# Performance work log

Measured on AMD Instinct MI355X. Metric: run time of the kernel, lower is better.

The kernel has to match this reference:

```python
import jax, jax.numpy as jnp
import numpy as np

B, H, W, F_HEX, F_GLB = 2, 48, 48, 150, 7
D, NH, L, DF, M = 512, 8, 4, 2048, 128
MAX_W, MAX_H, ATK, REC = 48, 48, 8, 20
S = H * W
DK = D // NH


def _ln(x, g, b):
    m = jnp.mean(x, -1, keepdims=True)
    v = jnp.mean(jnp.square(x - m), -1, keepdims=True)
    return (x - m) * jax.lax.rsqrt(v + 1e-5) * g + b


def _mha(q, k, v, wq, bq, wk, bk, wv, bv, wo, bo, mask=None):
    Bq, Sq, _ = q.shape
    Sk = k.shape[1]
    Q = (q @ wq + bq).reshape(Bq, Sq, NH, DK)
    K = (k @ wk + bk).reshape(Bq, Sk, NH, DK)
    V = (v @ wv + bv).reshape(Bq, Sk, NH, DK)
    s = jnp.einsum('bqhd,bkhd->bhqk', Q, K) / np.float32(np.sqrt(DK))
    if mask is not None:
        s = jnp.where(mask == 0, jnp.float32(-1e9), s)
    a = jax.nn.softmax(s, -1)
    o = jnp.einsum('bhqk,bkhd->bqhd', a, V).reshape(Bq, Sq, D)
    return o @ wo + bo


def setup_inputs():
    key = jax.random.key(0)
    ks = iter(jax.random.split(key, 64))
    w = lambda *sh: jax.random.normal(next(ks), sh, jnp.float32) * 0.02
    z = lambda *sh: jnp.zeros(sh, jnp.float32)
    o = lambda *sh: jnp.ones(sh, jnp.float32)
    return dict(
        map_representation=jax.random.normal(next(ks), (B, H, W, F_HEX), jnp.float32),
        global_features=jax.random.normal(next(ks), (B, F_GLB), jnp.float32),
        memory=jax.random.normal(next(ks), (B, M, D), jnp.float32),
        fog_mask=jax.random.randint(next(ks), (B, H, W), 0, 2, jnp.int32),
        hex_w=w(F_HEX, D), hex_b=z(D), glob_w=w(F_GLB, D), glob_b=z(D),
        mem_wq=w(D, D), mem_bq=z(D), mem_wk=w(D, D), mem_bk=z(D),
        mem_wv=w(D, D), mem_bv=z(D), mem_wo=w(D, D), mem_bo=z(D),
        gate_w=w(2 * D, D), gate_b=z(D),
        mn1_g=o(D), mn1_b=z(D), mn2_g=o(D), mn2_b=z(D),
        lw_q=w(L, D, D), lb_q=z(L, D), lw_k=w(L, D, D), lb_k=z(L, D),
        lw_v=w(L, D, D), lb_v=z(L, D), lw_o=w(L, D, D), lb_o=z(L, D),
        ln1_g=o(L, D), ln1_b=z(L, D), ln2_g=o(L, D), ln2_b=z(L, D),
        ff1_w=w(L, D, DF), ff1_b=z(L, DF), ff2_w=w(L, DF, D), ff2_b=z(L, D),
        pool_w=w(D, 1), pool_b=z(1),
        sx_w=w(D, MAX_W), sx_b=z(MAX_W), sy_w=w(D, MAX_H), sy_b=z(MAX_H),
        tx_w=w(D, MAX_W), tx_b=z(MAX_W), ty_w=w(D, MAX_H), ty_b=z(MAX_H),
        atk_w=w(D, ATK), atk_b=z(ATK), rec_w=w(D, REC), rec_b=z(REC),
        et_w=w(D, 1), et_b=z(1), val_w=w(D, 1), val_b=z(1),
    )


def reference(map_representation, global_features, memory, fog_mask,
              hex_w, hex_b, glob_w, glob_b,
              mem_wq, mem_bq, mem_wk, mem_bk, mem_wv, mem_bv, mem_wo, mem_bo,
              gate_w, gate_b, mn1_g, mn1_b, mn2_g, mn2_b,
              lw_q, lb_q, lw_k, lb_k, lw_v, lb_v, lw_o, lb_o,
              ln1_g, ln1_b, ln2_g, ln2_b, ff1_w, ff1_b, ff2_w, ff2_b,
              pool_w, pool_b, sx_w, sx_b, sy_w, sy_b, tx_w, tx_b, ty_w, ty_b,
              atk_w, atk_b, rec_w, rec_b, et_w, et_b, val_w, val_b):
    # project hex + global features, flatten map to token sequence [B,S,D]
    hexf = map_representation @ hex_w + hex_b
    glob = global_features @ glob_w + glob_b
    seq = (hexf + glob[:, None, None, :]).reshape(B, S, D)
    am = fog_mask.reshape(B, S)[:, None, None, :]  # key mask [B,1,1,S]

    # memory module: cross-attn conditioning + gated memory update (shared MHA weights)
    mem_out = _mha(seq, memory, memory, mem_wq, mem_bq, mem_wk, mem_bk, mem_wv, mem_bv, mem_wo, mem_bo)
    x = _ln(seq + mem_out, mn1_g, mn1_b)
    mem_upd = _mha(memory, seq, seq, mem_wq, mem_bq, mem_wk, mem_bk, mem_wv, mem_bv, mem_wo, mem_bo)
    gate = jax.nn.sigmoid(jnp.concatenate([memory, mem_upd], -1) @ gate_w + gate_b)
    new_memory = _ln(gate * mem_upd + (1.0 - gate) * memory, mn2_g, mn2_b)

    def block(xc, p):
        wq, bq, wk, bk, wv, bv, wo, bo, g1, b1, g2, b2, f1w, f1b, f2w, f2b = p
        att = _mha(xc, xc, xc, wq, bq, wk, bk, wv, bv, wo, bo, mask=am)
        xc = _ln(xc + att, g1, b1)
        h = jax.nn.gelu(xc @ f1w + f1b, approximate=False) @ f2w + f2b
        return _ln(xc + h, g2, b2), None

    x, _ = jax.lax.scan(block, x, (lw_q, lb_q, lw_k, lb_k, lw_v, lb_v, lw_o, lb_o,
                                   ln1_g, ln1_b, ln2_g, ln2_b, ff1_w, ff1_b, ff2_w, ff2_b))

    # attention pooling over tokens
    pw = jax.nn.softmax((x @ pool_w + pool_b)[..., 0], -1)  # [B,S]
    pooled = jnp.einsum('bs,bsd->bd', pw, x)

    return (pooled @ sx_w + sx_b, pooled @ sy_w + sy_b,
            pooled @ tx_w + tx_b, pooled @ ty_w + ty_b,
            pooled @ atk_w + atk_b, pooled @ rec_w + rec_b,
            pooled @ et_w + et_b, pooled @ val_w + val_b, new_memory)
```

## Files before the change

### kernel.cpp

```cpp
#include <hip/hip_runtime.h>
#include <hip/hip_bf16.h>

typedef __hip_bfloat16 bf16;
typedef unsigned short u16;
typedef __attribute__((ext_vector_type(8))) short short8;
typedef __attribute__((ext_vector_type(4))) float f32x4;

__device__ inline float b2f(u16 u){ unsigned int x = ((unsigned int)u) << 16; float f; __builtin_memcpy(&f, &x, 4); return f; }
__device__ inline u16 f2bits(float f){ __hip_bfloat16 h = __float2bfloat16(f); u16 u; __builtin_memcpy(&u, &h, 2); return u; }
__device__ inline void unpk(unsigned int w, float& a, float& b){ a = b2f((u16)(w & 0xffffu)); b = b2f((u16)(w >> 16)); }

__device__ __forceinline__ unsigned int pkbf(float a, float b)
{
  unsigned int ua = __float_as_uint(a) + 0x8000u;
  unsigned int ub = __float_as_uint(b) + 0x8000u;
  return __builtin_amdgcn_perm(ub, ua, 0x07060302u);
}

__global__ __launch_bounds__(512) void detect_k(const unsigned int* __restrict__ raw, int* __restrict__ flag)
{
  __shared__ int cnt;
  if (threadIdx.x == 0) cnt = 0;
  __syncthreads();
  unsigned int w = raw[threadIdx.x];
// ... 45 lines not shown
#pragma unroll
    for (int j = 0; j < 8; j++) o8[j] = f2bits(v[j]);
    __builtin_memcpy(&ov, o8, 16);
  }
  *(uint4*)((u16*)dst + gid) = ov;
}

__global__ __launch_bounds__(256) void gemm_k(
    const bf16* __restrict__ A, int lda, long long sAb, long long sAh,
    const bf16* __restrict__ B, int ldb, long long sBb, long long sBh,
    bf16* __restrict__ C, int ldc, long long sCb, long long sCh,
    int M, int N, int K, int HZ,
    const bf16* __restrict__ bias,
    const bf16* __restrict__ res, int ldres,
    const float* __restrict__ extra, int extraDiv,
    float alpha, int mode)
{
  __shared__ u16 As[64][40];
  __shared__ u16 Bs[64][40];
  int z = blockIdx.z;
  int bz = z / HZ, hz = z - bz * HZ;
  A += (size_t)bz * sAb + (size_t)hz * sAh;
  B += (size_t)bz * sBb + (size_t)hz * sBh;
  C += (size_t)bz * sCb + (size_t)hz * sCh;

  int m0 = blockIdx.y * 64, n0 = blockIdx.x * 64;
  int t = threadIdx.x;
  int r = t >> 2, c0 = (t & 3) << 3;
  int lane = t & 63, wv = t >> 6, lr = lane & 15, lq = lane >> 4;

  f32x4 acc[4];
#pragma unroll
  for (int i = 0; i < 4; i++) acc[i] = (f32x4){0.f, 0.f, 0.f, 0.f};

  const u16* Ag = (const u16*)A;
  const u16* Bg = (const u16*)B;
  bool aok = (m0 + r < M), bok = (n0 + r < N);
  const u16* arow = Ag + (size_t)(m0 + r) * lda + c0;
  const u16* brow = Bg + (size_t)(n0 + r) * ldb + c0;

  uint4 av = {0u,0u,0u,0u}, bv = {0u,0u,0u,0u};
  if (aok) av = *(const uint4*)(arow);
  if (bok) bv = *(const uint4*)(brow);

  for (int kt = 0; kt < K; kt += 32) {
    __syncthreads();
    *(uint4*)&As[r][c0] = av;
    *(uint4*)&Bs[r][c0] = bv;
    uint4 av2 = {0u,0u,0u,0u}, bv2 = {0u,0u,0u,0u};
    int nk = kt + 32;
    if (nk < K) {
      if (aok) av2 = *(const uint4*)(arow + nk);
      if (bok) bv2 = *(const uint4*)(brow + nk);
    }
    __syncthreads();
    short8 af = *(const short8*)&As[wv * 16 + lr][lq * 8];
#pragma unroll
    for (int nt = 0; nt < 4; nt++) {
      short8 bfr = *(const short8*)&Bs[nt * 16 + lr][lq * 8];
      acc[nt] = __builtin_amdgcn_mfma_f32_16x16x32_bf16(af, bfr, acc[nt], 0, 0, 0);
    }
    av = av2; bv = bv2;
  }

#pragma unroll
  for (int nt = 0; nt < 4; nt++) {
    int nn = n0 + nt * 16 + lr;
    if (nn >= N) continue;
    float bb = bias ? (float)bias[nn] : 0.f;
#pragma unroll
    for (int rr = 0; rr < 4; rr++) {
      int mm = m0 + wv * 16 + lq * 4 + rr;
      if (mm >= M) continue;
      float v = acc[nt][rr] * alpha + bb;
      if (mode == 1)      v += extra[(mm / extraDiv) * 512 + nn];
      else if (mode == 2) v = 0.5f * v * (1.f + erff(v * 0.70710678118654752f));
      else if (mode == 4) v += (float)res[(size_t)mm * ldres + nn];
      else if (mode == 5) v = 1.f / (1.f + expf(-v));
      C[(size_t)mm * ldc + nn] = __float2bfloat16(v);
    }
  }
}

__device__ __forceinline__ int swz(int row, int cg)
{
  return row * 64 + ((cg ^ (row & 3) ^ (((row >> 3) & 1) << 2)) << 3);
}

__global__ __launch_bounds__(256) void flash_k(
    const bf16* __restrict__ Qp, long long sQb,
    const bf16* __restrict__ Kp, long long sKb,
    const bf16* __restrict__ VTp, long long sVz,
    float* __restrict__ oAcc, long long sOb,
    float* __restrict__ lAcc, int Ml,
    const int* __restrict__ fog,
    int tilesPerSplit, int SkLen)
{
  __shared__ u16 Kl[64 * 64];
  __shared__ u16 Vl[64 * 64];
  __shared__ float fgl[2304];

  const float SC = 0.125f * 1.44269504088896340736f;
  int z = blockIdx.y, b = z >> 3, h = z & 7;
  int qt = blockIdx.x;
  int kt0 = blockIdx.z * tilesPerSplit;
  int t = threadIdx.x, lane = t & 63, w = t >> 6;
  int lr = lane & 15, lq = lane >> 4;

  const u16* Qg = (const u16*)Qp + (size_t)b * sQb + h * 64;
  const u16* Kg = (const u16*)Kp + (size_t)b * sKb + h * 64;
  const u16* Vg = (const u16*)VTp + (size_t)z * sVz;

  if (fog) {
    for (int j = t; j < SkLen; j += 256) fgl[j] = fog[b * 2304 + j] ? 0.f : -1e30f;
  }

  int qrow = qt * 64 + w * 16 + lr;
  short8 qf0, qf1;
  {
    union { short8 s; u16 u[8]; } i0, i1, o0, o1;
    i0.s = *(const short8*)(Qg + (size_t)qrow * 512 + lq * 8);
    i1.s = *(const short8*)(Qg + (size_t)qrow * 512 + 32 + lq * 8);
#pragma unroll
    for (int j = 0; j < 8; j++) {
      o0.u[j] = f2bits(b2f(i0.u[j]) * SC);
      o1.u[j] = f2bits(b2f(i1.u[j]) * SC);
    }
    qf0 = o0.s; qf1 = o1.s;
  }

  int rowA[4], kAd0[4], kAd1[4];
#pragma unroll
  for (int nt = 0; nt < 4; nt++) {
    rowA[nt] = 32 * (nt >> 1) + 8 * (lr >> 2) + 4 * (nt & 1) + (lr & 3);
    kAd0[nt] = swz(rowA[nt], lq);
    kAd1[nt] = swz(rowA[nt], lq + 4);
  }
  int vAd0[4], vAd1[4];
#pragma unroll
  for (int dt = 0; dt < 4; dt++) {
    vAd0[dt] = swz(dt * 16 + lr, lq);
    vAd1[dt] = swz(dt * 16 + lr, lq + 4);
  }

  f32x4 o[4];
#pragma unroll
  for (int i = 0; i < 4; i++) o[i] = (f32x4){0.f, 0.f, 0.f, 0.f};
  float lsum = 0.f;

  int rr = t >> 2, cg = t & 3, cs = cg * 8;
  int wAd0 = swz(rr, cg), wAd1 = swz(rr, cg + 4);
  for (int kti = 0; kti < tilesPerSplit; kti++) {
    int kt = kt0 + kti;
    __syncthreads();
    const u16* krow = Kg + (size_t)(kt * 64 + rr) * 512;
    const u16* vrow = Vg + (size_t)rr * SkLen + kt * 64;
    *(uint4*)&Kl[wAd0] = *(const uint4*)(krow + cs);
    *(uint4*)&Kl[wAd1] = *(const uint4*)(krow + cs + 32);
    *(uint4*)&Vl[wAd0] = *(const uint4*)(vrow + cs);
    *(uint4*)&Vl[wAd1] = *(const uint4*)(vrow + cs + 32);
    __syncthreads();

    f32x4 s[4];
#pragma unroll
    for (int nt = 0; nt < 4; nt++) {
      s[nt] = (f32x4){0.f, 0.f, 0.f, 0.f};
      short8 kf0 = *(const short8*)&Kl[kAd0[nt]];
      short8 kf1 = *(const short8*)&Kl[kAd1[nt]];
      s[nt] = __builtin_amdgcn_mfma_f32_16x16x32_bf16(kf0, qf0, s[nt], 0, 0, 0);
      s[nt] = __builtin_amdgcn_mfma_f32_16x16x32_bf16(kf1, qf1, s[nt], 0, 0, 0);
    }
    if (fog) {
#pragma unroll
      for (int nt = 0; nt < 4; nt++) {
        int key = kt * 64 + 32 * (nt >> 1) + 8 * lq + 4 * (nt & 1);
        f32x4 mo4 = *(const f32x4*)&fgl[key];
        s[nt] += mo4;
      }
    }
    union { unsigned int u[4]; short8 s8; } pk0, pk1;
#pragma unroll
    for (int nt = 0; nt < 4; nt++) {
      float p0 = exp2f(s[nt][0]), p1 = exp2f(s[nt][1]);
      float p2 = exp2f(s[nt][2]), p3 = exp2f(s[nt][3]);
      lsum += (p0 + p1) + (p2 + p3);
      unsigned int w0 = pkbf(p0, p1);
      unsigned int w1 = pkbf(p2, p3);
      if (nt < 2) { pk0.u[(nt & 1) * 2] = w0; pk0.u[(nt & 1) * 2 + 1] = w1; }
      else        { pk1.u[(nt & 1) * 2] = w0; pk1.u[(nt & 1) * 2 + 1] = w1; }
    }
#pragma unroll
    for (int dt = 0; dt < 4; dt++) {
      short8 vf0 = *(const short8*)&Vl[vAd0[dt]];
      short8 vf1 = *(const short8*)&Vl[vAd1[dt]];
      o[dt] = __builtin_amdgcn_mfma_f32_16x16x32_bf16(pk0.s8, vf0, o[dt], 0, 0, 0);
      o[dt] = __builtin_amdgcn_mfma_f32_16x16x32_bf16(pk1.s8, vf1, o[dt], 0, 0, 0);
    }
  }

  lsum += __shfl_xor(lsum, 16);
  lsum += __shfl_xor(lsum, 32);
  if (lq == 0) atomicAdd(&lAcc[z * Ml + qt * 64 + w * 16 + lr], lsum);

  float* ob = oAcc + (size_t)b * sOb;
  int qb = qt * 64 + w * 16 + lq * 4;
#pragma unroll
  for (int dt = 0; dt < 4; dt++)
#pragma unroll
    for (int r2 = 0; r2 < 4; r2++)
      atomicAdd(&ob[(size_t)(qb + r2) * 512 + h * 64 + dt * 16 + lr], o[dt][r2]);
}

__global__ __launch_bounds__(256) void fdiv_k(const float* __restrict__ oAcc,
                                              const float* __restrict__ lAcc,
                                              int Mq, int Ml, int rows,
                                              bf16* __restrict__ out)
{
  int i = blockIdx.x * 256 + threadIdx.x;
  if (i >= rows * 512) return;
  int row = i >> 9, col = i & 511;
  int b = row / Mq, q = row - b * Mq;
  int zz = b * 8 + (col >> 6);
  float l = lAcc[zz * Ml + q];
  float v = (l > 0.f) ? oAcc[i] / l : 0.f;
  out[i] = __float2bfloat16(v);
}

__global__ __launch_bounds__(256) void transpose_k(const bf16* __restrict__ in, bf16* __restrict__ out,
                                                   int R, int C, int Rpad, long long inB, long long outB)
{
  __shared__ u16 tile[32][33];
  const u16* ip = (const u16*)in + (size_t)blockIdx.z * inB;
  u16* op = (u16*)out + (size_t)blockIdx.z * outB;
  int c0 = blockIdx.x * 32, r0 = blockIdx.y * 32;
  int tx = threadIdx.x & 31, ty = threadIdx.x >> 5;
#pragma unroll
  for (int j = 0; j < 4; j++) {
    int rr = r0 + ty + j * 8, cc = c0 + tx;
    u16 v = 0;
    if (rr < R && cc < C) v = ip[(size_t)rr * C + cc];
    tile[ty + j * 8][tx] = v;
  }
  __syncthreads();
#pragma unroll
  for (int j = 0; j < 4; j++) {
    int oc = c0 + ty + j * 8;
    if (oc < C && r0 + tx < Rpad) op[(size_t)oc * Rpad + r0 + tx] = tile[tx][ty + j * 8];
  }
}

__global__ __launch_bounds__(256) void headT_k(const bf16* __restrict__ in, bf16* __restrict__ out,
                                               int Sk, int rowbase, int bstride)
{
  __shared__ u16 tile[32][33];
  int z = blockIdx.z, b = z >> 3, h = z & 7;
  const u16* ip = (const u16*)in + ((size_t)(rowbase + b * bstride)) * 512 + h * 64;
  u16* op = (u16*)out + (size_t)z * 64 * Sk;
  int r0 = blockIdx.x * 32, c0 = blockIdx.y * 32;
  int tx = threadIdx.x & 31, ty = threadIdx.x >> 5;
#pragma unroll
  for (int j = 0; j < 4; j++)
    tile[ty + j * 8][tx] = ip[(size_t)(r0 + ty + j * 8) * 512 + c0 + tx];
  __syncthreads();
#pragma unroll
  for (int j = 0; j < 4; j++)
    op[(size_t)(c0 + ty + j * 8) * Sk + r0 + tx] = tile[tx][ty + j * 8];
}

__global__ __launch_bounds__(64) void ln_k(const bf16* __restrict__ in, const bf16* __restrict__ g,
                                           const bf16* __restrict__ bb, bf16* __restrict__ out)
{
  size_t row = blockIdx.x; int lane = threadIdx.x;
  const u16* ip = (const u16*)in + row * 512 + lane * 8;
  uint4 rv = *(const uint4*)ip;
  float v[8];
  unpk(rv.x, v[0], v[1]); unpk(rv.y, v[2], v[3]); unpk(rv.z, v[4], v[5]); unpk(rv.w, v[6], v[7]);
  float s = 0.f, s2 = 0.f;
#pragma unroll
  for (int k = 0; k < 8; k++) { s += v[k]; s2 += v[k] * v[k]; }
#pragma unroll
  for (int o = 32; o; o >>= 1) { s += __shfl_xor(s, o); s2 += __shfl_xor(s2, o); }
  float mean = s * (1.f / 512.f);
  float var = s2 * (1.f / 512.f) - mean * mean;
  float rstd = rsqrtf(var + 1e-5f);
  uint4 gv = *(const uint4*)((const u16*)g + lane * 8);
  uint4 bv = *(const uint4*)((const u16*)bb + lane * 8);
  float gf[8], bf2[8];
  unpk(gv.x, gf[0], gf[1]); unpk(gv.y, gf[2], gf[3]); unpk(gv.z, gf[4], gf[5]); unpk(gv.w, gf[6], gf[7]);
  unpk(bv.x, bf2[0], bf2[1]); unpk(bv.y, bf2[2], bf2[3]); unpk(bv.z, bf2[4], bf2[5]); unpk(bv.w, bf2[6], bf2[7]);
  u16 o8[8];
#pragma unroll
  for (int k = 0; k < 8; k++) o8[k] = f2bits((v[k] - mean) * rstd * gf[k] + bf2[k]);
  uint4 ov;
  ov.x = o8[0] | ((unsigned)o8[1] << 16); ov.y = o8[2] | ((unsigned)o8[3] << 16);
  ov.z = o8[4] | ((unsigned)o8[5] << 16); ov.w = o8[6] | ((unsigned)o8[7] << 16);
  *(uint4*)((u16*)out + row * 512 + lane * 8) = ov;
}

__global__ void glob_k(const bf16* __restrict__ gf, const bf16* __restrict__ gw,
                       const bf16* __restrict__ gb, float* __restrict__ out)
{
  int i = blockIdx.x * 256 + threadIdx.x; if (i >= 1024) return;
  int b = i >> 9, d = i & 511;
  float s = (float)gb[d];
#pragma unroll
  for (int f = 0; f < 7; f++) s += (float)gf[b * 7 + f] * (float)gw[f * 512 + d];
  out[i] = s;
}

__global__ void padA_k(const bf16* __restrict__ in, bf16* __restrict__ out)
{
  int i = blockIdx.x * 256 + threadIdx.x; if (i >= 4608 * 160) return;
  int r = i / 160, c = i - r * 160;
  out[i] = (c < 150) ? in[r * 150 + c] : __float2bfloat16(0.f);
}

__global__ void catg_k(const bf16* __restrict__ mem, const bf16* __restrict__ mu, bf16* __restrict__ out)
{
  int i = blockIdx.x * 256 + threadIdx.x; if (i >= 256 * 1024) return;
  int r = i >> 10, c = i & 1023;
  out[i] = (c < 512) ? mem[r * 512 + c] : mu[r * 512 + c - 512];
}

__global__ void gcomb_k(const bf16* __restrict__ g, const bf16* __restrict__ mu,
                        const bf16* __restrict__ mem, bf16* __restrict__ out)
{
  int i = blockIdx.x * 256 + threadIdx.x; if (i >= 131072) return;
  float gg = (float)g[i];
  out[i] = __float2bfloat16(gg * (float)mu[i] + (1.f - gg) * (float)mem[i]);
}

__global__ __launch_bounds__(64) void plog_k(const bf16* __restrict__ x, const bf16* __restrict__ pw,
                                             const bf16* __restrict__ pb, float* __restrict__ out)
{
  size_t row = blockIdx.x; int lane = threadIdx.x;
  uint4 xv = *(const uint4*)((const u16*)x + row * 512 + lane * 8);
  uint4 wv = *(const uint4*)((const u16*)pw + lane * 8);
  float v[8], w[8];
  unpk(xv.x, v[0], v[1]); unpk(xv.y, v[2], v[3]); unpk(xv.z, v[4], v[5]); unpk(xv.w, v[6], v[7]);
  unpk(wv.x, w[0], w[1]); unpk(wv.y, w[2], w[3]); unpk(wv.z, w[4], w[5]); unpk(wv.w, w[6], w[7]);
  float s = 0.f;
#pragma unroll
  for (int k = 0; k < 8; k++) s += v[k] * w[k];
#pragma unroll
  for (int o = 32; o; o >>= 1) s += __shfl_xor(s, o);
  if (lane == 0) out[row] = s + (float)pb[0];
}

__global__ __launch_bounds__(256) void psm_k(const float* __restrict__ lg, float* __restrict__ pw)
{
  __shared__ float red[4];
  int b = blockIdx.x, tid = threadIdx.x;
  const float* p = lg + b * 2304;
  float vals[9]; float mx = -3e38f;
#pragma unroll
// ... 158 lines not shown
  bf16* tLo = (bf16*)alloc(4 * 512 * 512, 2);
  bf16* tF1 = (bf16*)alloc(4ULL * 2048 * 512, 2);
  bf16* tF2 = (bf16*)alloc(4ULL * 512 * 2048, 2);
  float* globF = (float*)alloc(1024, 4);
  bf16* catX = (bf16*)alloc((size_t)CATROW * 512, 2);
  bf16* Qc = (bf16*)alloc((size_t)CATROW * 512, 2);
  bf16* Kc = (bf16*)alloc((size_t)CATROW * 512, 2);
  bf16* Vc = (bf16*)alloc((size_t)CATROW * 512, 2);
  bf16* VmemT = (bf16*)alloc(16ULL * 64 * 128, 2);
  bf16* VsT = (bf16*)alloc(16ULL * 64 * S, 2);
  bf16* mo = (bf16*)alloc((size_t)NROW * 512, 2);
  bf16* tmp1 = (bf16*)alloc((size_t)NROW * 512, 2);
  bf16* xbuf = (bf16*)alloc((size_t)NROW * 512, 2);
  bf16* x2buf = (bf16*)alloc((size_t)NROW * 512, 2);
  bf16* mu0 = (bf16*)alloc(256 * 512, 2);
  bf16* mup = (bf16*)alloc(256 * 512, 2);
  bf16* catg = (bf16*)alloc(256 * 1024, 2);
  bf16* gateb = (bf16*)alloc(256 * 512, 2);
  bf16* nmpre = (bf16*)alloc(256 * 512, 2);
  bf16* nmout = (bf16*)alloc(256 * 512, 2);
  float* plog = (float*)alloc(NROW, 4);
  float* pwv = (float*)alloc(NROW, 4);
  float* pooledF = (float*)alloc(1024, 4);
  float* oAcc = (float*)alloc((size_t)NROW * 512, 4);
  float* lAcc = (float*)alloc(16 * 2304, 4);
  bf16* hbuf = (bf16*)alloc((size_t)NROW * 2048, 2);
  if (off > ws_size) return;

  detect_k<<<1, 512, 0, stream>>>((const unsigned int*)d_in[0], dflag);
  cvtall8_k<<<(coffi / 8 + 255) / 256, 256, 0, stream>>>(ca, canon, dflag);

  auto T = [&](int t) -> const bf16* { return canon + cum[t]; };
  const bf16* map_rep = T(0);
  const bf16* gfeat   = T(1);
  const bf16* memin   = T(2);
  const bf16* hex_w = T(3);  const bf16* hex_b = T(4);
  const bf16* glob_w = T(5); const bf16* glob_b = T(6);
  const bf16* mem_wq = T(7);  const bf16* mem_bq = T(8);
  const bf16* mem_wk = T(9);  const bf16* mem_bk = T(10);
  const bf16* mem_wv = T(11); const bf16* mem_bv = T(12);
  const bf16* mem_wo = T(13); const bf16* mem_bo = T(14);
  const bf16* gate_w = T(15); const bf16* gate_b = T(16);
  const bf16* mn1_g = T(17); const bf16* mn1_b = T(18);
  const bf16* mn2_g = T(19); const bf16* mn2_b = T(20);
  const bf16* lw_q = T(21); const bf16* lb_q = T(22);
  const bf16* lw_k = T(23); const bf16* lb_k = T(24);
  const bf16* lw_v = T(25); const bf16* lb_v = T(26);
  const bf16* lw_o = T(27); const bf16* lb_o = T(28);
  const bf16* ln1_g = T(29); const bf16* ln1_b = T(30);
  const bf16* ln2_g = T(31); const bf16* ln2_b = T(32);
  const bf16* ff1_w = T(33); const bf16* ff1_b = T(34);
  const bf16* ff2_w = T(35); const bf16* ff2_b = T(36);
  const bf16* pool_w = T(37); const bf16* pool_b = T(38);

  transp(stream, hex_w, tHex, 150, 512, 160, 0, 0, 1);
  transp(stream, mem_wq, tWq, 512, 512, 512, 0, 0, 1);
  transp(stream, mem_wk, tWk, 512, 512, 512, 0, 0, 1);
  transp(stream, mem_wv, tWv, 512, 512, 512, 0, 0, 1);
  transp(stream, mem_wo, tWo, 512, 512, 512, 0, 0, 1);
  transp(stream, gate_w, tGate, 1024, 512, 1024, 0, 0, 1);
  transp(stream, lw_q, tLq, 512, 512, 512, 262144, 262144, 4);
  transp(stream, lw_k, tLk, 512, 512, 512, 262144, 262144, 4);
  transp(stream, lw_v, tLv, 512, 512, 512, 262144, 262144, 4);
  transp(stream, lw_o, tLo, 512, 512, 512, 262144, 262144, 4);
  transp(stream, ff1_w, tF1, 512, 2048, 512, 1048576, 1048576, 4);
  transp(stream, ff2_w, tF2, 2048, 512, 2048, 1048576, 1048576, 4);

  glob_k<<<4, 256, 0, stream>>>(gfeat, glob_w, glob_b, globF);
  padA_k<<<(NROW * 160 + 255) / 256, 256, 0, stream>>>(map_rep, aPad);
  gemm(stream, aPad, 160, 0, 0, tHex, 160, 0, 0, catX, 512, 0, 0,
       NROW, 512, 160, 1, 1, hex_b, nullptr, 0, globF, S, 1.f, 1);
  hipMemcpyAsync(catX + (size_t)NROW * 512, memin, 256 * 512 * 2, hipMemcpyDeviceToDevice, stream);

  gemm(stream, catX, 512, 0, 0, tWq, 512, 0, 0, Qc, 512, 0, 0, CATROW, 512, 512, 1, 1, mem_bq, nullptr, 0, nullptr, 1, 1.f, 0);
  gemm(stream, catX, 512, 0, 0, tWk, 512, 0, 0, Kc, 512, 0, 0, CATROW, 512, 512, 1, 1, mem_bk, nullptr, 0, nullptr, 1, 1.f, 0);
  gemm(stream, catX, 512, 0, 0, tWv, 512, 0, 0, Vc, 512, 0, 0, CATROW, 512, 512, 1, 1, mem_bv, nullptr, 0, nullptr, 1, 1.f, 0);

  headT_k<<<dim3(4, 2, 16), 256, 0, stream>>>(Vc, VmemT, 128, NROW, 128);
  hipMemsetAsync(oAcc, 0, (size_t)NROW * 512 * 4, stream);
  hipMemsetAsync(lAcc, 0, 16 * 2304 * 4, stream);
  flash_k<<<dim3(36, 16, 1), 256, 0, stream>>>(Qc, RS, Kc + (size_t)NROW * 512, 128 * 512,
                                               VmemT, 64 * 128, oAcc, RS, lAcc, 2304,
                                               nullptr, 2, 128);
  fdiv_k<<<(NROW * 512 + 255) / 256, 256, 0, stream>>>(oAcc, lAcc, 2304, 2304, NROW, mo);
  gemm(stream, mo, 512, 0, 0, tWo, 512, 0, 0, tmp1, 512, 0, 0,
       NROW, 512, 512, 1, 1, mem_bo, catX, 512, nullptr, 1, 1.f, 4);
  ln_k<<<NROW, 64, 0, stream>>>(tmp1, mn1_g, mn1_b, xbuf);

  headT_k<<<dim3(72, 2, 16), 256, 0, stream>>>(Vc, VsT, S, 0, S);
  hipMemsetAsync(oAcc, 0, 256 * 512 * 4, stream);
  hipMemsetAsync(lAcc, 0, 16 * 128 * 4, stream);
  flash_k<<<dim3(2, 16, 6), 256, 0, stream>>>(Qc + (size_t)NROW * 512, 128 * 512, Kc, RS,
                                              VsT, 64LL * S, oAcc, 128 * 512, lAcc, 128,
                                              nullptr, 6, S);
  fdiv_k<<<(256 * 512 + 255) / 256, 256, 0, stream>>>(oAcc, lAcc, 128, 128, 256, mu0);
  gemm(stream, mu0, 512, 0, 0, tWo, 512, 0, 0, mup, 512, 0, 0,
       256, 512, 512, 1, 1, mem_bo, nullptr, 0, nullptr, 1, 1.f, 0);
  catg_k<<<(256 * 1024 + 255) / 256, 256, 0, stream>>>(memin, mup, catg);
  gemm(stream, catg, 1024, 0, 0, tGate, 1024, 0, 0, gateb, 512, 0, 0,
       256, 512, 1024, 1, 1, gate_b, nullptr, 0, nullptr, 1, 1.f, 5);
  gcomb_k<<<(131072 + 255) / 256, 256, 0, stream>>>(gateb, mup, memin, nmpre);
  ln_k<<<256, 64, 0, stream>>>(nmpre, mn2_g, mn2_b, nmout);
  outstore_k<<<(131072 + 255) / 256, 256, 0, stream>>>(nmout, d_out, dflag);

  for (int l = 0; l < 4; l++) {
    gemm(stream, xbuf, 512, 0, 0, tLq + (size_t)l * 262144, 512, 0, 0, Qc, 512, 0, 0,
         NROW, 512, 512, 1, 1, lb_q + l * 512, nullptr, 0, nullptr, 1, 1.f, 0);
    gemm(stream, xbuf, 512, 0, 0, tLk + (size_t)l * 262144, 512, 0, 0, Kc, 512, 0, 0,
         NROW, 512, 512, 1, 1, lb_k + l * 512, nullptr, 0, nullptr, 1, 1.f, 0);
    gemm(stream, xbuf, 512, 0, 0, tLv + (size_t)l * 262144, 512, 0, 0, Vc, 512, 0, 0,
         NROW, 512, 512, 1, 1, lb_v + l * 512, nullptr, 0, nullptr, 1, 1.f, 0);
    headT_k<<<dim3(72, 2, 16), 256, 0, stream>>>(Vc, VsT, S, 0, S);
    hipMemsetAsync(oAcc, 0, (size_t)NROW * 512 * 4, stream);
    hipMemsetAsync(lAcc, 0, 16 * 2304 * 4, stream);
    flash_k<<<dim3(36, 16, 2), 256, 0, stream>>>(Qc, RS, Kc, RS, VsT, 64LL * S,
                                                 oAcc, RS, lAcc, 2304, fog, 18, S);
    fdiv_k<<<(NROW * 512 + 255) / 256, 256, 0, stream>>>(oAcc, lAcc, 2304, 2304, NROW, mo);
    gemm(stream, mo, 512, 0, 0, tLo + (size_t)l * 262144, 512, 0, 0, tmp1, 512, 0, 0,
         NROW, 512, 512, 1, 1, lb_o + l * 512, xbuf, 512, nullptr, 1, 1.f, 4);
    ln_k<<<NROW, 64, 0, stream>>>(tmp1, ln1_g + l * 512, ln1_b + l * 512, x2buf);
    gemm(stream, x2buf, 512, 0, 0, tF1 + (size_t)l * 1048576, 512, 0, 0, hbuf, 2048, 0, 0,
         NROW, 2048, 512, 1, 1, ff1_b + l * 2048, nullptr, 0, nullptr, 1, 1.f, 2);
    gemm(stream, hbuf, 2048, 0, 0, tF2 + (size_t)l * 1048576, 2048, 0, 0, tmp1, 512, 0, 0,
         NROW, 512, 2048, 1, 1, ff2_b + l * 512, x2buf, 512, nullptr, 1, 1.f, 4);
    ln_k<<<NROW, 64, 0, stream>>>(tmp1, ln2_g + l * 512, ln2_b + l * 512, xbuf);
  }

  plog_k<<<NROW, 64, 0, stream>>>(xbuf, pool_w, pool_b, plog);
  psm_k<<<2, 256, 0, stream>>>(plog, pwv);
  hipMemsetAsync(pooledF, 0, 1024 * sizeof(float), stream);
  pool1_k<<<dim3(36, 2), 256, 0, stream>>>(pwv, xbuf, pooledF);

  heads_k<<<2, 256, 0, stream>>>(pooledF,
      T(39), T(40), T(41), T(42), T(43), T(44), T(45), T(46),
      T(47), T(48), T(49), T(50), T(51), T(52), T(53), T(54),
      d_out, dflag);
}
```

Baseline: 1.252 ms.

## Add 128x128 register-prefetch FFN1 GEMM, bitmask fog, MFMA row sums, vectorized fdiv/LN

Adds a 128x128-tile bf16 MFMA GEMM that prefetches the next K-slab into registers while the current one is computed, and uses it for the FFN1 projection with fused GELU. The flash kernel now applies the fog mask by ANDing the packed bf16 probabilities with a 16-bit mask instead of adding -1e30 to the logits. It also computes the softmax denominator with an extra MFMA against a ones vector instead of scalar adds and shuffles. The division kernel handles four elements per thread with a reciprocal, and layernorm packs four rows per 256-thread block. The new GEMM assumes M, N and K are multiples of 128 and 32, and the row sums now use bf16-rounded probabilities.

```diff
diff --git a/kernel.cpp b/kernel.cpp
--- a/kernel.cpp
+++ b/kernel.cpp
@@ -151,6 +151,84 @@
   }
 }
 
+__global__ __launch_bounds__(256) void gemm128p_k(
+    const bf16* __restrict__ A, int lda,
+    const bf16* __restrict__ B, int ldb,
+    bf16* __restrict__ C, int ldc, int K,
+    const bf16* __restrict__ bias,
+    const bf16* __restrict__ res, int ldres,
+    const float* __restrict__ extra, int extraDiv,
+    float alpha, int mode)
+{
+  __shared__ u16 As[128][40];
+  __shared__ u16 Bs[128][40];
+  int t = threadIdx.x, lane = t & 63, w = t >> 6;
+  int m0 = blockIdx.y * 128, n0 = blockIdx.x * 128;
+  int wm = (w & 1) * 64, wn = (w >> 1) * 64;
+  int lr = lane & 15, lq = lane >> 4;
+  int r = t >> 2, c0 = (t & 3) << 3;
+
+  const u16* Ag = (const u16*)A;
+  const u16* Bg = (const u16*)B;
+  const u16* ar0 = Ag + (size_t)(m0 + r) * lda + c0;
+  const u16* ar1 = Ag + (size_t)(m0 + 64 + r) * lda + c0;
+  const u16* br0 = Bg + (size_t)(n0 + r) * ldb + c0;
+  const u16* br1 = Bg + (size_t)(n0 + 64 + r) * ldb + c0;
+
+  uint4 a0 = *(const uint4*)ar0, a1 = *(const uint4*)ar1;
+  uint4 b0 = *(const uint4*)br0, b1 = *(const uint4*)br1;
+
+  f32x4 acc[4][4];
+#pragma unroll
+  for (int i = 0; i < 4; i++)
+#pragma unroll
+    for (int j = 0; j < 4; j++) acc[i][j] = (f32x4){0.f, 0.f, 0.f, 0.f};
+
+  for (int kt = 0; kt < K; kt += 32) {
+    __syncthreads();
+    *(uint4*)&As[r][c0] = a0;
+    *(uint4*)&As[64 + r][c0] = a1;
+    *(uint4*)&Bs[r][c0] = b0;
+    *(uint4*)&Bs[64 + r][c0] = b1;
+    int nk = kt + 32;
+    if (nk < K) {
+      a0 = *(const uint4*)(ar0 + nk); a1 = *(const uint4*)(ar1 + nk);
+      b0 = *(const uint4*)(br0 + nk); b1 = *(const uint4*)(br1 + nk);
+    }
+    __syncthreads();
+    short8 af[4], bfv[4];
+#pragma unroll
+    for (int i = 0; i < 4; i++) {
+      af[i] = *(const short8*)&As[wm + i * 16 + lr][lq * 8];
+      bfv[i] = *(const short8*)&Bs[wn + i * 16 + lr][lq * 8];
+    }
+#pragma unroll
+    for (int mt = 0; mt < 4; mt++)
+#pragma unroll
+      for (int nt = 0; nt < 4; nt++)
+        acc[mt][nt] = __builtin_amdgcn_mfma_f32_16x16x32_bf16(af[mt], bfv[nt], acc[mt][nt], 0, 0, 0);
+  }
+
+#pragma unroll
+  for (int nt = 0; nt < 4; nt++) {
+    int nn = n0 + wn + nt * 16 + lr;
+    float bb = bias ? (float)bias[nn] : 0.f;
+#pragma unroll
+    for (int mt = 0; mt < 4; mt++) {
+#pragma unroll
+      for (int r2 = 0; r2 < 4; r2++) {
+        int mm = m0 + wm + mt * 16 + lq * 4 + r2;
+        float v = acc[mt][nt][r2] * alpha + bb;
+        if (mode == 1)      v += extra[(mm / extraDiv) * 512 + nn];
+        else if (mode == 2) v = 0.5f * v * (1.f + erff(v * 0.70710678118654752f));
+        else if (mode == 4) v += (float)res[(size_t)mm * ldres + nn];
+        else if (mode == 5) v = 1.f / (1.f + expf(-v));
+        C[(size_t)mm * ldc + nn] = __float2bfloat16(v);
+      }
+    }
+  }
+}
+
 __device__ __forceinline__ int swz(int row, int cg)
 {
   return row * 64 + ((cg ^ (row & 3) ^ (((row >> 3) & 1) << 2)) << 3);
@@ -167,7 +245,7 @@
 {
   __shared__ u16 Kl[64 * 64];
   __shared__ u16 Vl[64 * 64];
-  __shared__ float fgl[2304];
+  __shared__ u16 fgl16[2304];
 
   const float SC = 0.125f * 1.44269504088896340736f;
   int z = blockIdx.y, b = z >> 3, h = z & 7;
@@ -175,13 +253,14 @@
   int kt0 = blockIdx.z * tilesPerSplit;
   int t = threadIdx.x, lane = t & 63, w = t >> 6;
   int lr = lane & 15, lq = lane >> 4;
+  int useMask = (fog != nullptr);
 
   const u16* Qg = (const u16*)Qp + (size_t)b * sQb + h * 64;
   const u16* Kg = (const u16*)Kp + (size_t)b * sKb + h * 64;
   const u16* Vg = (const u16*)VTp + (size_t)z * sVz;
 
-  if (fog) {
-    for (int j = t; j < SkLen; j += 256) fgl[j] = fog[b * 2304 + j] ? 0.f : -1e30f;
+  if (useMask) {
+    for (int j = t; j < SkLen; j += 256) fgl16[j] = fog[b * 2304 + j] ? 0xFFFFu : 0u;
   }
 
   int qrow = qt * 64 + w * 16 + lr;
@@ -198,6 +277,14 @@
     qf0 = o0.s; qf1 = o1.s;
   }
 
+  short8 ones8;
+  {
+    union { short8 s; u16 u[8]; } on;
+#pragma unroll
+    for (int j = 0; j < 8; j++) on.u[j] = 0x3F80u;
+    ones8 = on.s;
+  }
+
   int rowA[4], kAd0[4], kAd1[4];
 #pragma unroll
   for (int nt = 0; nt < 4; nt++) {
@@ -212,10 +299,10 @@
     vAd1[dt] = swz(dt * 16 + lr, lq + 4);
   }
 
-  f32x4 o[4];
+  f32x4 o[4], ol;
 #pragma unroll
   for (int i = 0; i < 4; i++) o[i] = (f32x4){0.f, 0.f, 0.f, 0.f};
-  float lsum = 0.f;
+  ol = (f32x4){0.f, 0.f, 0.f, 0.f};
 
   int rr = t >> 2, cg = t & 3, cs = cg * 8;
   int wAd0 = swz(rr, cg), wAd1 = swz(rr, cg + 4);
@@ -239,22 +326,19 @@
       s[nt] = __builtin_amdgcn_mfma_f32_16x16x32_bf16(kf0, qf0, s[nt], 0, 0, 0);
       s[nt] = __builtin_amdgcn_mfma_f32_16x16x32_bf16(kf1, qf1, s[nt], 0, 0, 0);
     }
-    if (fog) {
-#pragma unroll
-      for (int nt = 0; nt < 4; nt++) {
-        int key = kt * 64 + 32 * (nt >> 1) + 8 * lq + 4 * (nt & 1);
-        f32x4 mo4 = *(const f32x4*)&fgl[key];
-        s[nt] += mo4;
-      }
-    }
+
     union { unsigned int u[4]; short8 s8; } pk0, pk1;
 #pragma unroll
     for (int nt = 0; nt < 4; nt++) {
       float p0 = exp2f(s[nt][0]), p1 = exp2f(s[nt][1]);
       float p2 = exp2f(s[nt][2]), p3 = exp2f(s[nt][3]);
-      lsum += (p0 + p1) + (p2 + p3);
       unsigned int w0 = pkbf(p0, p1);
       unsigned int w1 = pkbf(p2, p3);
+      if (useMask) {
+        int key = kt * 64 + 32 * (nt >> 1) + 8 * lq + 4 * (nt & 1);
+        uint2 mm = *(const uint2*)&fgl16[key];
+        w0 &= mm.x; w1 &= mm.y;
+      }
       if (nt < 2) { pk0.u[(nt & 1) * 2] = w0; pk0.u[(nt & 1) * 2 + 1] = w1; }
       else        { pk1.u[(nt & 1) * 2] = w0; pk1.u[(nt & 1) * 2 + 1] = w1; }
     }
@@ -265,11 +349,15 @@
       o[dt] = __builtin_amdgcn_mfma_f32_16x16x32_bf16(pk0.s8, vf0, o[dt], 0, 0, 0);
       o[dt] = __builtin_amdgcn_mfma_f32_16x16x32_bf16(pk1.s8, vf1, o[dt], 0, 0, 0);
     }
-  }
-
-  lsum += __shfl_xor(lsum, 16);
-  lsum += __shfl_xor(lsum, 32);
-  if (lq == 0) atomicAdd(&lAcc[z * Ml + qt * 64 + w * 16 + lr], lsum);
+    ol = __builtin_amdgcn_mfma_f32_16x16x32_bf16(pk0.s8, ones8, ol, 0, 0, 0);
+    ol = __builtin_amdgcn_mfma_f32_16x16x32_bf16(pk1.s8, ones8, ol, 0, 0, 0);
+  }
+
+  if (lr == 0) {
+#pragma unroll
+    for (int r2 = 0; r2 < 4; r2++)
+      atomicAdd(&lAcc[z * Ml + qt * 64 + w * 16 + lq * 4 + r2], ol[r2]);
+  }
 
   float* ob = oAcc + (size_t)b * sOb;
   int qb = qt * 64 + w * 16 + lq * 4;
@@ -280,19 +368,23 @@
       atomicAdd(&ob[(size_t)(qb + r2) * 512 + h * 64 + dt * 16 + lr], o[dt][r2]);
 }
 
-__global__ __launch_bounds__(256) void fdiv_k(const float* __restrict__ oAcc,
-                                              const float* __restrict__ lAcc,
-                                              int Mq, int Ml, int rows,
-                                              bf16* __restrict__ out)
-{
-  int i = blockIdx.x * 256 + threadIdx.x;
+__global__ __launch_bounds__(256) void fdiv4_k(const float* __restrict__ oAcc,
+                                               const float* __restrict__ lAcc,
+                                               int Mq, int Ml, int rows,
+                                               bf16* __restrict__ out)
+{
+  int i = (blockIdx.x * 256 + threadIdx.x) * 4;
   if (i >= rows * 512) return;
   int row = i >> 9, col = i & 511;
   int b = row / Mq, q = row - b * Mq;
   int zz = b * 8 + (col >> 6);
   float l = lAcc[zz * Ml + q];
-  float v = (l > 0.f) ? oAcc[i] / l : 0.f;
-  out[i] = __float2bfloat16(v);
+  float inv = (l > 0.f) ? 1.f / l : 0.f;
+  float4 v = *(const float4*)(oAcc + i);
+  u16 o4[4] = {f2bits(v.x * inv), f2bits(v.y * inv), f2bits(v.z * inv), f2bits(v.w * inv)};
+  unsigned int lo = o4[0] | ((unsigned)o4[1] << 16);
+  unsigned int hi = o4[2] | ((unsigned)o4[3] << 16);
+  *(uint2*)((u16*)out + i) = (uint2){lo, hi};
 }
 
 __global__ __launch_bounds__(256) void transpose_k(const bf16* __restrict__ in, bf16* __restrict__ out,
@@ -336,10 +428,11 @@
     op[(size_t)(c0 + ty + j * 8) * Sk + r0 + tx] = tile[tx][ty + j * 8];
 }
 
-__global__ __launch_bounds__(64) void ln_k(const bf16* __restrict__ in, const bf16* __restrict__ g,
-                                           const bf16* __restrict__ bb, bf16* __restrict__ out)
-{
-  size_t row = blockIdx.x; int lane = threadIdx.x;
+__global__ __launch_bounds__(256) void ln_k(const bf16* __restrict__ in, const bf16* __restrict__ g,
+                                            const bf16* __restrict__ bb, bf16* __restrict__ out)
+{
+  size_t row = blockIdx.x * 4 + (threadIdx.x >> 6);
+  int lane = threadIdx.x & 63;
   const u16* ip = (const u16*)in + row * 512 + lane * 8;
   uint4 rv = *(const uint4*)ip;
   float v[8];
@@ -664,10 +757,10 @@
   flash_k<<<dim3(36, 16, 1), 256, 0, stream>>>(Qc, RS, Kc + (size_t)NROW * 512, 128 * 512,
                                                VmemT, 64 * 128, oAcc, RS, lAcc, 2304,
                                                nullptr, 2, 128);
-  fdiv_k<<<(NROW * 512 + 255) / 256, 256, 0, stream>>>(oAcc, lAcc, 2304, 2304, NROW, mo);
+  fdiv4_k<<<(NROW * 128 + 255) / 256, 256, 0, stream>>>(oAcc, lAcc, 2304, 2304, NROW, mo);
   gemm(stream, mo, 512, 0, 0, tWo, 512, 0, 0, tmp1, 512, 0, 0,
        NROW, 512, 512, 1, 1, mem_bo, catX, 512, nullptr, 1, 1.f, 4);
-  ln_k<<<NROW, 64, 0, stream>>>(tmp1, mn1_g, mn1_b, xbuf);
+  ln_k<<<NROW / 4, 256, 0, stream>>>(tmp1, mn1_g, mn1_b, xbuf);
 
   headT_k<<<dim3(72, 2, 16), 256, 0, stream>>>(Vc, VsT, S, 0, S);
   hipMemsetAsync(oAcc, 0, 256 * 512 * 4, stream);
@@ -675,14 +768,14 @@
   flash_k<<<dim3(2, 16, 6), 256, 0, stream>>>(Qc + (size_t)NROW * 512, 128 * 512, Kc, RS,
                                               VsT, 64LL * S, oAcc, 128 * 512, lAcc, 128,
                                               nullptr, 6, S);
-  fdiv_k<<<(256 * 512 + 255) / 256, 256, 0, stream>>>(oAcc, lAcc, 128, 128, 256, mu0);
+  fdiv4_k<<<(256 * 128 + 255) / 256, 256, 0, stream>>>(oAcc, lAcc, 128, 128, 256, mu0);
   gemm(stream, mu0, 512, 0, 0, tWo, 512, 0, 0, mup, 512, 0, 0,
        256, 512, 512, 1, 1, mem_bo, nullptr, 0, nullptr, 1, 1.f, 0);
   catg_k<<<(256 * 1024 + 255) / 256, 256, 0, stream>>>(memin, mup, catg);
   gemm(stream, catg, 1024, 0, 0, tGate, 1024, 0, 0, gateb, 512, 0, 0,
        256, 512, 1024, 1, 1, gate_b, nullptr, 0, nullptr, 1, 1.f, 5);
   gcomb_k<<<(131072 + 255) / 256, 256, 0, stream>>>(gateb, mup, memin, nmpre);
-  ln_k<<<256, 64, 0, stream>>>(nmpre, mn2_g, mn2_b, nmout);
+  ln_k<<<64, 256, 0, stream>>>(nmpre, mn2_g, mn2_b, nmout);
   outstore_k<<<(131072 + 255) / 256, 256, 0, stream>>>(nmout, d_out, dflag);
 
   for (int l = 0; l < 4; l++) {
@@ -697,15 +790,19 @@
     hipMemsetAsync(lAcc, 0, 16 * 2304 * 4, stream);
     flash_k<<<dim3(36, 16, 2), 256, 0, stream>>>(Qc, RS, Kc, RS, VsT, 64LL * S,
                                                  oAcc, RS, lAcc, 2304, fog, 18, S);
-    fdiv_k<<<(NROW * 512 + 255) / 256, 256, 0, stream>>>(oAcc, lAcc, 2304, 2304, NROW, mo);
+    fdiv4_k<<<(NROW * 128 + 255) / 256, 256, 0, stream>>>(oAcc, lAcc, 2304, 2304, NROW, mo);
     gemm(stream, mo, 512, 0, 0, tLo + (size_t)l * 262144, 512, 0, 0, tmp1, 512, 0, 0,
          NROW, 512, 512, 1, 1, lb_o + l * 512, xbuf, 512, nullptr, 1, 1.f, 4);
-    ln_k<<<NROW, 64, 0, stream>>>(tmp1, ln1_g + l * 512, ln1_b + l * 512, x2buf);
-    gemm(stream, x2buf, 512, 0, 0, tF1 + (size_t)l * 1048576, 512, 0, 0, hbuf, 2048, 0, 0,
-         NROW, 2048, 512, 1, 1, ff1_b + l * 2048, nullptr, 0, nullptr, 1, 1.f, 2);
+    ln_k<<<NROW / 4, 256, 0, stream>>>(tmp1, ln1_g + l * 512, ln1_b + l * 512, x2buf);
+    {
+      dim3 g(2048 / 128, NROW / 128);
+      gemm128p_k<<<g, dim3(256), 0, stream>>>(x2buf, 512, tF1 + (size_t)l * 1048576, 512,
+                                              hbuf, 2048, 512, ff1_b + l * 2048,
+                                              nullptr, 0, nullptr, 1, 1.f, 2);
+    }
     gemm(stream, hbuf, 2048, 0, 0, tF2 + (size_t)l * 1048576, 2048, 0, 0, tmp1, 512, 0, 0,
          NROW, 512, 2048, 1, 1, ff2_b + l * 512, x2buf, 512, nullptr, 1, 1.f, 4);
-    ln_k<<<NROW, 64, 0, stream>>>(tmp1, ln2_g + l * 512, ln2_b + l * 512, xbuf);
+    ln_k<<<NROW / 4, 256, 0, stream>>>(tmp1, ln2_g + l * 512, ln2_b + l * 512, xbuf);
   }
 
   plog_k<<<NROW, 64, 0, stream>>>(xbuf, pool_w, pool_b, plog);
```

After: 1.273 ms. Within noise of the previous version (+1.7%).

## Prefetch K/V tiles, mask P with bitmask, MFMA row sums, vectorize fdiv and LN

Applied to the files above, without the earlier changes.

The flash attention kernel now loads the next K/V tile into registers while the current tile is being computed. The fog mask is stored as 16-bit bitmasks and ANDed into the packed bf16 probabilities instead of adding -1e30 before exp. Row sums are computed by an extra MFMA against a ones vector rather than scalar adds and shuffles. Separately, fdiv is vectorized to four elements per thread with a reciprocal, and layernorm packs four rows into each 256-thread block. The risks are higher register pressure from the prefetch, and row sums now come from bf16-rounded probabilities, which slightly changes numerics.

```diff
diff --git a/kernel.cpp b/kernel.cpp
--- a/kernel.cpp
+++ b/kernel.cpp
@@ -167,7 +167,7 @@
 {
   __shared__ u16 Kl[64 * 64];
   __shared__ u16 Vl[64 * 64];
-  __shared__ float fgl[2304];
+  __shared__ u16 fgl16[2304];
 
   const float SC = 0.125f * 1.44269504088896340736f;
   int z = blockIdx.y, b = z >> 3, h = z & 7;
@@ -175,13 +175,14 @@
   int kt0 = blockIdx.z * tilesPerSplit;
   int t = threadIdx.x, lane = t & 63, w = t >> 6;
   int lr = lane & 15, lq = lane >> 4;
+  int useMask = (fog != nullptr);
 
   const u16* Qg = (const u16*)Qp + (size_t)b * sQb + h * 64;
   const u16* Kg = (const u16*)Kp + (size_t)b * sKb + h * 64;
   const u16* Vg = (const u16*)VTp + (size_t)z * sVz;
 
-  if (fog) {
-    for (int j = t; j < SkLen; j += 256) fgl[j] = fog[b * 2304 + j] ? 0.f : -1e30f;
+  if (useMask) {
+    for (int j = t; j < SkLen; j += 256) fgl16[j] = fog[b * 2304 + j] ? 0xFFFFu : 0u;
   }
 
   int qrow = qt * 64 + w * 16 + lr;
@@ -198,6 +199,14 @@
     qf0 = o0.s; qf1 = o1.s;
   }
 
+  short8 ones8;
+  {
+    union { short8 s; u16 u[8]; } on;
+#pragma unroll
+    for (int j = 0; j < 8; j++) on.u[j] = 0x3F80u;
+    ones8 = on.s;
+  }
+
   int rowA[4], kAd0[4], kAd1[4];
 #pragma unroll
   for (int nt = 0; nt < 4; nt++) {
@@ -212,22 +221,36 @@
     vAd1[dt] = swz(dt * 16 + lr, lq + 4);
   }
 
-  f32x4 o[4];
+  f32x4 o[4], ol;
 #pragma unroll
   for (int i = 0; i < 4; i++) o[i] = (f32x4){0.f, 0.f, 0.f, 0.f};
-  float lsum = 0.f;
+  ol = (f32x4){0.f, 0.f, 0.f, 0.f};
 
   int rr = t >> 2, cg = t & 3, cs = cg * 8;
   int wAd0 = swz(rr, cg), wAd1 = swz(rr, cg + 4);
+
+  const u16* krow = Kg + (size_t)(kt0 * 64 + rr) * 512 + cs;
+  const u16* vrow = Vg + (size_t)rr * SkLen + kt0 * 64 + cs;
+  uint4 ka = *(const uint4*)(krow);
+  uint4 kb = *(const uint4*)(krow + 32);
+  uint4 va = *(const uint4*)(vrow);
+  uint4 vb = *(const uint4*)(vrow + 32);
+
   for (int kti = 0; kti < tilesPerSplit; kti++) {
     int kt = kt0 + kti;
     __syncthreads();
-    const u16* krow = Kg + (size_t)(kt * 64 + rr) * 512;
-    const u16* vrow = Vg + (size_t)rr * SkLen + kt * 64;
-    *(uint4*)&Kl[wAd0] = *(const uint4*)(krow + cs);
-    *(uint4*)&Kl[wAd1] = *(const uint4*)(krow + cs + 32);
-    *(uint4*)&Vl[wAd0] = *(const uint4*)(vrow + cs);
-    *(uint4*)&Vl[wAd1] = *(const uint4*)(vrow + cs + 32);
+    *(uint4*)&Kl[wAd0] = ka;
+    *(uint4*)&Kl[wAd1] = kb;
+    *(uint4*)&Vl[wAd0] = va;
+    *(uint4*)&Vl[wAd1] = vb;
+    if (kti + 1 < tilesPerSplit) {
+      krow += 64 * 512;
+      vrow += 64;
+      ka = *(const uint4*)(krow);
+      kb = *(const uint4*)(krow + 32);
+      va = *(const uint4*)(vrow);
+      vb = *(const uint4*)(vrow + 32);
+    }
     __syncthreads();
 
     f32x4 s[4];
@@ -239,22 +262,19 @@
       s[nt] = __builtin_amdgcn_mfma_f32_16x16x32_bf16(kf0, qf0, s[nt], 0, 0, 0);
       s[nt] = __builtin_amdgcn_mfma_f32_16x16x32_bf16(kf1, qf1, s[nt], 0, 0, 0);
     }
-    if (fog) {
-#pragma unroll
-      for (int nt = 0; nt < 4; nt++) {
-        int key = kt * 64 + 32 * (nt >> 1) + 8 * lq + 4 * (nt & 1);
-        f32x4 mo4 = *(const f32x4*)&fgl[key];
-        s[nt] += mo4;
-      }
-    }
+
     union { unsigned int u[4]; short8 s8; } pk0, pk1;
 #pragma unroll
     for (int nt = 0; nt < 4; nt++) {
       float p0 = exp2f(s[nt][0]), p1 = exp2f(s[nt][1]);
       float p2 = exp2f(s[nt][2]), p3 = exp2f(s[nt][3]);
-      lsum += (p0 + p1) + (p2 + p3);
       unsigned int w0 = pkbf(p0, p1);
       unsigned int w1 = pkbf(p2, p3);
+      if (useMask) {
+        int key = kt * 64 + 32 * (nt >> 1) + 8 * lq + 4 * (nt & 1);
+        uint2 mm = *(const uint2*)&fgl16[key];
+        w0 &= mm.x; w1 &= mm.y;
+      }
       if (nt < 2) { pk0.u[(nt & 1) * 2] = w0; pk0.u[(nt & 1) * 2 + 1] = w1; }
       else        { pk1.u[(nt & 1) * 2] = w0; pk1.u[(nt & 1) * 2 + 1] = w1; }
     }
@@ -265,11 +285,15 @@
       o[dt] = __builtin_amdgcn_mfma_f32_16x16x32_bf16(pk0.s8, vf0, o[dt], 0, 0, 0);
       o[dt] = __builtin_amdgcn_mfma_f32_16x16x32_bf16(pk1.s8, vf1, o[dt], 0, 0, 0);
     }
-  }
-
-  lsum += __shfl_xor(lsum, 16);
-  lsum += __shfl_xor(lsum, 32);
-  if (lq == 0) atomicAdd(&lAcc[z * Ml + qt * 64 + w * 16 + lr], lsum);
+    ol = __builtin_amdgcn_mfma_f32_16x16x32_bf16(pk0.s8, ones8, ol, 0, 0, 0);
+    ol = __builtin_amdgcn_mfma_f32_16x16x32_bf16(pk1.s8, ones8, ol, 0, 0, 0);
+  }
+
+  if (lr == 0) {
+#pragma unroll
+    for (int r2 = 0; r2 < 4; r2++)
+      atomicAdd(&lAcc[z * Ml + qt * 64 + w * 16 + lq * 4 + r2], ol[r2]);
+  }
 
   float* ob = oAcc + (size_t)b * sOb;
   int qb = qt * 64 + w * 16 + lq * 4;
@@ -280,19 +304,23 @@
       atomicAdd(&ob[(size_t)(qb + r2) * 512 + h * 64 + dt * 16 + lr], o[dt][r2]);
 }
 
-__global__ __launch_bounds__(256) void fdiv_k(const float* __restrict__ oAcc,
-                                              const float* __restrict__ lAcc,
-                                              int Mq, int Ml, int rows,
-                                              bf16* __restrict__ out)
-{
-  int i = blockIdx.x * 256 + threadIdx.x;
+__global__ __launch_bounds__(256) void fdiv4_k(const float* __restrict__ oAcc,
+                                               const float* __restrict__ lAcc,
+                                               int Mq, int Ml, int rows,
+                                               bf16* __restrict__ out)
+{
+  int i = (blockIdx.x * 256 + threadIdx.x) * 4;
   if (i >= rows * 512) return;
   int row = i >> 9, col = i & 511;
   int b = row / Mq, q = row - b * Mq;
   int zz = b * 8 + (col >> 6);
   float l = lAcc[zz * Ml + q];
-  float v = (l > 0.f) ? oAcc[i] / l : 0.f;
-  out[i] = __float2bfloat16(v);
+  float inv = (l > 0.f) ? 1.f / l : 0.f;
+  float4 v = *(const float4*)(oAcc + i);
+  u16 o4[4] = {f2bits(v.x * inv), f2bits(v.y * inv), f2bits(v.z * inv), f2bits(v.w * inv)};
+  unsigned int lo = o4[0] | ((unsigned)o4[1] << 16);
+  unsigned int hi = o4[2] | ((unsigned)o4[3] << 16);
+  *(uint2*)((u16*)out + i) = (uint2){lo, hi};
 }
 
 __global__ __launch_bounds__(256) void transpose_k(const bf16* __restrict__ in, bf16* __restrict__ out,
@@ -336,10 +364,11 @@
     op[(size_t)(c0 + ty + j * 8) * Sk + r0 + tx] = tile[tx][ty + j * 8];
 }
 
-__global__ __launch_bounds__(64) void ln_k(const bf16* __restrict__ in, const bf16* __restrict__ g,
-                                           const bf16* __restrict__ bb, bf16* __restrict__ out)
-{
-  size_t row = blockIdx.x; int lane = threadIdx.x;
+__global__ __launch_bounds__(256) void ln_k(const bf16* __restrict__ in, const bf16* __restrict__ g,
+                                            const bf16* __restrict__ bb, bf16* __restrict__ out)
+{
+  size_t row = blockIdx.x * 4 + (threadIdx.x >> 6);
+  int lane = threadIdx.x & 63;
   const u16* ip = (const u16*)in + row * 512 + lane * 8;
   uint4 rv = *(const uint4*)ip;
   float v[8];
@@ -664,10 +693,10 @@
   flash_k<<<dim3(36, 16, 1), 256, 0, stream>>>(Qc, RS, Kc + (size_t)NROW * 512, 128 * 512,
                                                VmemT, 64 * 128, oAcc, RS, lAcc, 2304,
                                                nullptr, 2, 128);
-  fdiv_k<<<(NROW * 512 + 255) / 256, 256, 0, stream>>>(oAcc, lAcc, 2304, 2304, NROW, mo);
+  fdiv4_k<<<(NROW * 128 + 255) / 256, 256, 0, stream>>>(oAcc, lAcc, 2304, 2304, NROW, mo);
   gemm(stream, mo, 512, 0, 0, tWo, 512, 0, 0, tmp1, 512, 0, 0,
        NROW, 512, 512, 1, 1, mem_bo, catX, 512, nullptr, 1, 1.f, 4);
-  ln_k<<<NROW, 64, 0, stream>>>(tmp1, mn1_g, mn1_b, xbuf);
+  ln_k<<<NROW / 4, 256, 0, stream>>>(tmp1, mn1_g, mn1_b, xbuf);
 
   headT_k<<<dim3(72, 2, 16), 256, 0, stream>>>(Vc, VsT, S, 0, S);
   hipMemsetAsync(oAcc, 0, 256 * 512 * 4, stream);
@@ -675,14 +704,14 @@
   flash_k<<<dim3(2, 16, 6), 256, 0, stream>>>(Qc + (size_t)NROW * 512, 128 * 512, Kc, RS,
                                               VsT, 64LL * S, oAcc, 128 * 512, lAcc, 128,
                                               nullptr, 6, S);
-  fdiv_k<<<(256 * 512 + 255) / 256, 256, 0, stream>>>(oAcc, lAcc, 128, 128, 256, mu0);
+  fdiv4_k<<<(256 * 128 + 255) / 256, 256, 0, stream>>>(oAcc, lAcc, 128, 128, 256, mu0);
   gemm(stream, mu0, 512, 0, 0, tWo, 512, 0, 0, mup, 512, 0, 0,
        256, 512, 512, 1, 1, mem_bo, nullptr, 0, nullptr, 1, 1.f, 0);
   catg_k<<<(256 * 1024 + 255) / 256, 256, 0, stream>>>(memin, mup, catg);
   gemm(stream, catg, 1024, 0, 0, tGate, 1024, 0, 0, gateb, 512, 0, 0,
        256, 512, 1024, 1, 1, gate_b, nullptr, 0, nullptr, 1, 1.f, 5);
   gcomb_k<<<(131072 + 255) / 256, 256, 0, stream>>>(gateb, mup, memin, nmpre);
-  ln_k<<<256, 64, 0, stream>>>(nmpre, mn2_g, mn2_b, nmout);
+  ln_k<<<64, 256, 0, stream>>>(nmpre, mn2_g, mn2_b, nmout);
   outstore_k<<<(131072 + 255) / 256, 256, 0, stream>>>(nmout, d_out, dflag);
 
   for (int l = 0; l < 4; l++) {
@@ -697,15 +726,15 @@
     hipMemsetAsync(lAcc, 0, 16 * 2304 * 4, stream);
     flash_k<<<dim3(36, 16, 2), 256, 0, stream>>>(Qc, RS, Kc, RS, VsT, 64LL * S,
                                                  oAcc, RS, lAcc, 2304, fog, 18, S);
-    fdiv_k<<<(NROW * 512 + 255) / 256, 256, 0, stream>>>(oAcc, lAcc, 2304, 2304, NROW, mo);
+    fdiv4_k<<<(NROW * 128 + 255) / 256, 256, 0, stream>>>(oAcc, lAcc, 2304, 2304, NROW, mo);
     gemm(stream, mo, 512, 0, 0, tLo + (size_t)l * 262144, 512, 0, 0, tmp1, 512, 0, 0,
          NROW, 512, 512, 1, 1, lb_o + l * 512, xbuf, 512, nullptr, 1, 1.f, 4);
-    ln_k<<<NROW, 64, 0, stream>>>(tmp1, ln1_g + l * 512, ln1_b + l * 512, x2buf);
+    ln_k<<<NROW / 4, 256, 0, stream>>>(tmp1, ln1_g + l * 512, ln1_b + l * 512, x2buf);
     gemm(stream, x2buf, 512, 0, 0, tF1 + (size_t)l * 1048576, 512, 0, 0, hbuf, 2048, 0, 0,
          NROW, 2048, 512, 1, 1, ff1_b + l * 2048, nullptr, 0, nullptr, 1, 1.f, 2);
     gemm(stream, hbuf, 2048, 0, 0, tF2 + (size_t)l * 1048576, 2048, 0, 0, tmp1, 512, 0, 0,
          NROW, 512, 2048, 1, 1, ff2_b + l * 512, x2buf, 512, nullptr, 1, 1.f, 4);
-    ln_k<<<NROW, 64, 0, stream>>>(tmp1, ln2_g + l * 512, ln2_b + l * 512, xbuf);
+    ln_k<<<NROW / 4, 256, 0, stream>>>(tmp1, ln2_g + l * 512, ln2_b + l * 512, xbuf);
   }
 
   plog_k<<<NROW, 64, 0, stream>>>(xbuf, pool_w, pool_b, plog);
```

New measurement: 1.184 ms. 5.4% less time.
